# Kernel optimization log

Measured on AMD Instinct MI355X. Metric: run time of the kernel, lower is better.

Reference implementation:

```python
import jax, jax.numpy as jnp
import numpy as np

B, S, D_IN, D_MODEL, H = 2, 2048, 1024, 1024, 16
HD = D_MODEL // H


def setup_inputs() -> dict:
    key = jax.random.key(0)
    ks = jax.random.split(key, 5)
    x = jax.random.normal(ks[0], (B, S, D_IN), dtype=jnp.float32)
    # nn.Linear default init scale ~ 1/sqrt(fan_in)
    w_qkv = jax.random.normal(ks[1], (D_IN, 3 * D_MODEL), dtype=jnp.float32) / np.sqrt(D_IN)
    b_qkv = jax.random.normal(ks[2], (3 * D_MODEL,), dtype=jnp.float32) * 0.02
    w_out = jax.random.normal(ks[3], (D_MODEL, D_MODEL), dtype=jnp.float32) / np.sqrt(D_MODEL)
    b_out = jax.random.normal(ks[4], (D_MODEL,), dtype=jnp.float32) * 0.02
    return {"x": x, "w_qkv": w_qkv, "b_qkv": b_qkv, "w_out": w_out, "b_out": b_out}


def reference(x, w_qkv, b_qkv, w_out, b_out):
    b, s, _ = x.shape
    qkv = x @ w_qkv + b_qkv                       # [b, s, 3*d_model]
    # per-head layout is [q_h | k_h | v_h]: reshape to (b, s, h, 3, hd)
    qkv = qkv.reshape(b, s, H, 3, HD).transpose(0, 2, 1, 3, 4)  # [b, h, s, 3, hd]
    q, k, v = qkv[..., 0, :], qkv[..., 1, :], qkv[..., 2, :]     # each [b, h, s, hd]
    scale = 1.0 / np.sqrt(HD).astype(np.float32)
    scores = jnp.einsum('bhqd,bhkd->bhqk', q, k) * scale         # [b, h, s, s]
    causal = jnp.tril(jnp.ones((s, s), dtype=bool))              # True = keep
    scores = jnp.where(causal, scores, -jnp.inf)
    attn = jax.nn.softmax(scores, axis=-1)
    out = jnp.einsum('bhqk,bhkd->bhqd', attn, v)                 # [b, h, s, hd]
    concat = out.transpose(0, 2, 1, 3).reshape(b, s, D_MODEL)
    return concat @ w_out + b_out
```

## Files before the change

kernel.cpp:

```cpp
#include <hip/hip_runtime.h>
#include <hip/hip_bf16.h>
#include <stdint.h>

typedef __attribute__((ext_vector_type(8))) short bf16x8;
typedef __attribute__((ext_vector_type(4))) float f32x4;

#define DEVFN static __device__ __forceinline__

typedef const __attribute__((address_space(1))) void* gas_ptr;
typedef __attribute__((address_space(3))) void* las_ptr;

DEVFN void async16(const void* g, void* l) {
  __builtin_amdgcn_global_load_lds((gas_ptr)g, (las_ptr)l, 16, 0, 0);
}

#define S_LEN 2048
#define NH    16
#define HDIM  64
#define KDIM  1024
#define NQKV  3072
#define MTOK  4096

#define QK_SCALE 0.1803368801111244f

__global__ __launch_bounds__(256) void prep_kernel(
    const float* __restrict__ x, const float* __restrict__ w_qkv,
    const float* __restrict__ w_out, __hip_bfloat16* __restrict__ xb,
    __hip_bfloat16* __restrict__ wqkt, __hip_bfloat16* __restrict__ wot) {
  __shared__ float T[64][65];
  const int j = blockIdx.x;
  const int tid = threadIdx.x;
  if (j < 2048) {
    const int i = (j * 256 + tid) * 8;
    float4 a = *(const float4*)(x + i);
    float4 b = *(const float4*)(x + i + 4);
    alignas(16) __hip_bfloat16 t[8] = {
        __float2bfloat16(a.x), __float2bfloat16(a.y),
        __float2bfloat16(a.z), __float2bfloat16(a.w),
        __float2bfloat16(b.x), __float2bfloat16(b.y),
        __float2bfloat16(b.z), __float2bfloat16(b.w)};
    *(uint4*)(xb + i) = *(const uint4*)t;
    return;
  }
  const float* in;
  __hip_bfloat16* out;
  int N, n0, k0;
  if (j < 2816) {
    const int j2 = j - 2048;
    in = w_qkv; out = wqkt; N = NQKV;
    n0 = (j2 % 48) * 64; k0 = (j2 / 48) * 64;
  } else {
    const int j3 = j - 2816;
    in = w_out; out = wot; N = KDIM;
    n0 = (j3 % 16) * 64; k0 = (j3 / 16) * 64;
  }
#pragma unroll
  for (int it = 0; it < 4; it++) {
    int r = it * 16 + (tid >> 4);
    int c = (tid & 15) * 4;
    float4 v = *(const float4*)&in[(size_t)(k0 + r) * N + n0 + c];
    T[r][c + 0] = v.x; T[r][c + 1] = v.y; T[r][c + 2] = v.z; T[r][c + 3] = v.w;
  }
  __syncthreads();
#pragma unroll
  for (int it = 0; it < 4; it++) {
    int rn = it * 16 + (tid >> 4);
    int ck = (tid & 15) * 4;
    alignas(8) __hip_bfloat16 t4[4];
#pragma unroll
    for (int jj = 0; jj < 4; jj++) t4[jj] = __float2bfloat16(T[ck + jj][rn]);
    *(ushort4*)&out[(size_t)(n0 + rn) * KDIM + k0 + ck] = *(const ushort4*)t4;
  }
}

__global__ __launch_bounds__(256, 2) void qkv_gemm_kernel(
    const __hip_bfloat16* __restrict__ A,
    const __hip_bfloat16* __restrict__ Bt,
    const float* __restrict__ bias,
    __hip_bfloat16* __restrict__ qo,
    __hip_bfloat16* __restrict__ ko,
    __hip_bfloat16* __restrict__ vto) {
  __shared__ __hip_bfloat16 As[2][128 * 32];
  __shared__ __hip_bfloat16 Bs[2][128 * 32];
  __shared__ __hip_bfloat16 Tb[4][16 * 72];
  const int tid = threadIdx.x;
  const int wave = tid >> 6, lane = tid & 63;
  const int L = lane & 15, quad = lane >> 4;
  const int wm = wave >> 1, wn = wave & 1;
  const int m0 = blockIdx.y * 128, n0 = blockIdx.x * 128;

  f32x4 acc[4][4] = {};

  const int srow = tid >> 2;
  const int scol = (tid & 3) * 8;
  const __hip_bfloat16* ag = A + (size_t)(m0 + srow) * KDIM + scol;
  const __hip_bfloat16* bg = Bt + (size_t)(n0 + srow) * KDIM + scol;
  char* asd0 = (char*)&As[0][0] + wave * 1024;
  char* asd1 = (char*)&As[1][0] + wave * 1024;
  char* bsd0 = (char*)&Bs[0][0] + wave * 1024;
  char* bsd1 = (char*)&Bs[1][0] + wave * 1024;

  for (int kt = 0; kt < KDIM; kt += 64) {
    async16(ag + kt, asd0);
    async16(ag + kt + (size_t)64 * KDIM, asd0 + 4096);
    async16(ag + kt + 32, asd1);
    async16(ag + kt + 32 + (size_t)64 * KDIM, asd1 + 4096);
    async16(bg + kt, bsd0);
    async16(bg + kt + (size_t)64 * KDIM, bsd0 + 4096);
    async16(bg + kt + 32, bsd1);
    async16(bg + kt + 32 + (size_t)64 * KDIM, bsd1 + 4096);
    __syncthreads();
    bf16x8 af[4][2], bf[4][2];
#pragma unroll
    for (int r = 0; r < 4; r++)
#pragma unroll
      for (int kd = 0; kd < 2; kd++)
        af[r][kd] = *(const bf16x8*)&As[kd][(wm * 64 + r * 16 + L) * 32 + quad * 8];
#pragma unroll
    for (int c = 0; c < 4; c++)
#pragma unroll
      for (int kd = 0; kd < 2; kd++)
        bf[c][kd] = *(const bf16x8*)&Bs[kd][(wn * 64 + c * 16 + L) * 32 + quad * 8];
#pragma unroll
    for (int r = 0; r < 4; r++)
#pragma unroll
      for (int c = 0; c < 4; c++) {
        acc[r][c] = __builtin_amdgcn_mfma_f32_16x16x32_bf16(af[r][0], bf[c][0],
                                                            acc[r][c], 0, 0, 0);
        acc[r][c] = __builtin_amdgcn_mfma_f32_16x16x32_bf16(af[r][1], bf[c][1],
                                                            acc[r][c], 0, 0, 0);
      }
    __syncthreads();
  }

  const int mbase = m0 + wm * 64;
  const int nbase = n0 + wn * 64;
  const int h = nbase / 192;
  const int t = (nbase % 192) / 64;
  const int b = mbase >> 11;
  const int s0 = mbase & 2047;
  __hip_bfloat16* Tw = &Tb[wave][0];
  float bv[4];
#pragma unroll
  for (int c = 0; c < 4; c++) bv[c] = bias[nbase + c * 16 + L];

  if (t == 2) {
#pragma unroll
    for (int c = 0; c < 4; c++) {
#pragma unroll
      for (int r = 0; r < 4; r++) {
        alignas(8) __hip_bfloat16 t4[4];
#pragma unroll
        for (int g = 0; g < 4; g++)
          t4[g] = __float2bfloat16(acc[r][c][g] + bv[c]);
        *(ushort4*)&Tw[L * 72 + r * 16 + quad * 4] = *(const ushort4*)t4;
      }
      __asm__ volatile("s_waitcnt lgkmcnt(0)" ::: "memory");
#pragma unroll
      for (int it = 0; it < 2; it++) {
        const int rr = it * 8 + (lane >> 3);
        const int cc = (lane & 7) * 8;
        uint4 u = *(const uint4*)&Tw[rr * 72 + cc];
        *(uint4*)&vto[((size_t)((b * NH + h) * HDIM + c * 16 + rr)) * S_LEN +
                      s0 + cc] = u;
      }
    }
  } else {
    __hip_bfloat16* dst = (t == 0) ? qo : ko;
    const float sc = (t == 0) ? QK_SCALE : 1.0f;
#pragma unroll
    for (int r = 0; r < 4; r++) {
#pragma unroll
      for (int c = 0; c < 4; c++)
#pragma unroll
        for (int g = 0; g < 4; g++)
          Tw[(quad * 4 + g) * 72 + c * 16 + L] =
              __float2bfloat16((acc[r][c][g] + bv[c]) * sc);
      __asm__ volatile("s_waitcnt lgkmcnt(0)" ::: "memory");
#pragma unroll
      for (int it = 0; it < 2; it++) {
        const int rr = it * 8 + (lane >> 3);
        const int cc = (lane & 7) * 8;
        uint4 u = *(const uint4*)&Tw[rr * 72 + cc];
        *(uint4*)&dst[((size_t)((b * NH + h) * S_LEN) + s0 + r * 16 + rr) *
                          HDIM + cc] = u;
      }
    }
  }
}

__global__ __launch_bounds__(256, 2) void flash_attn_kernel(
    const __hip_bfloat16* __restrict__ q,
    const __hip_bfloat16* __restrict__ k,
    const __hip_bfloat16* __restrict__ vt,
    __hip_bfloat16* __restrict__ attn) {
  __shared__ __hip_bfloat16 Ps[4][16 * 72];
  const int tid = threadIdx.x;
  const int wave = tid >> 6, lane = tid & 63;
  const int L = lane & 15, quad = lane >> 4;

  const int j = blockIdx.x;
  const int x = j & 7;
  const int c = (j >> 3) & 31;
  const int rr = j >> 8;
  const int bh = ((c & 3) << 3) + x;
  const int p = c >> 2;
  const int qi = rr ? p : (15 - p);
  const int qb = qi * 128;

  const __hip_bfloat16* Qg = q + (size_t)bh * S_LEN * HDIM;
  const __hip_bfloat16* Kg = k + (size_t)bh * S_LEN * HDIM;
  const __hip_bfloat16* Vg = vt + (size_t)bh * HDIM * S_LEN;

  int wq[2];
  wq[0] = qb + wave * 16;
  wq[1] = qb + 64 + wave * 16;

  bf16x8 qf[2][2];
#pragma unroll
  for (int r = 0; r < 2; r++)
#pragma unroll
    for (int kd = 0; kd < 2; kd++)
      qf[r][kd] =
          *(const bf16x8*)&Qg[(size_t)(wq[r] + L) * HDIM + kd * 32 + quad * 8];

  float l_i[2] = {0.f, 0.f};
  f32x4 o[2][4] = {};

  bf16x8 kc[4][2], kn[4][2];
#pragma unroll
  for (int ks = 0; ks < 4; ks++)
#pragma unroll
    for (int kd = 0; kd < 2; kd++)
      kc[ks][kd] =
          *(const bf16x8*)&Kg[(size_t)(ks * 16 + L) * HDIM + kd * 32 + quad * 8];

  const int nkt = 2 * (qi + 1);
  for (int kt = 0; kt < nkt; kt++) {
    const int k0 = kt * 64;
    bf16x8 vfr[4][2];
#pragma unroll
    for (int dsb = 0; dsb < 4; dsb++)
#pragma unroll
      for (int kf = 0; kf < 2; kf++)
        vfr[dsb][kf] = *(const bf16x8*)&Vg[(size_t)(dsb * 16 + L) * S_LEN + k0 +
                                           kf * 32 + quad * 8];

    f32x4 st[2][4] = {};
#pragma unroll
    for (int r = 0; r < 2; r++)
#pragma unroll
      for (int ks = 0; ks < 4; ks++)
#pragma unroll
        for (int kd = 0; kd < 2; kd++)
          st[r][ks] = __builtin_amdgcn_mfma_f32_16x16x32_bf16(
              kc[ks][kd], qf[r][kd], st[r][ks], 0, 0, 0);

    if (kt + 1 < nkt) {
      const int k1 = k0 + 64;
#pragma unroll
      for (int ks = 0; ks < 4; ks++)
#pragma unroll
        for (int kd = 0; kd < 2; kd++)
          kn[ks][kd] = *(const bf16x8*)&Kg[(size_t)(k1 + ks * 16 + L) * HDIM +
                                           kd * 32 + quad * 8];
    }

#pragma unroll
    for (int r = 0; r < 2; r++) {
      if (k0 > wq[r] + 15) continue;
      const int qrow = wq[r] + L;
      if (k0 + 63 > wq[r]) {
#pragma unroll
        for (int ks = 0; ks < 4; ks++)
#pragma unroll
          for (int g = 0; g < 4; g++) {
            int kk = k0 + ks * 16 + quad * 4 + g;
            if (kk > qrow) st[r][ks][g] = -1e30f;
          }
      }
      float rs = 0.f;
#pragma unroll
      for (int ks = 0; ks < 4; ks++) {
        f32x4 pv;
#pragma unroll
        for (int g = 0; g < 4; g++) {
          pv[g] = __builtin_amdgcn_exp2f(st[r][ks][g]);
          rs += pv[g];
        }
        alignas(8) __hip_bfloat16 t4[4];
#pragma unroll
        for (int g = 0; g < 4; g++) t4[g] = __float2bfloat16(pv[g]);
        *(ushort4*)&Ps[wave][L * 72 + ks * 16 + quad * 4] = *(const ushort4*)t4;
      }
      l_i[r] += rs;
      __asm__ volatile("s_waitcnt lgkmcnt(0)" ::: "memory");
      bf16x8 pf[2];
#pragma unroll
      for (int kf = 0; kf < 2; kf++)
        pf[kf] = *(const bf16x8*)&Ps[wave][L * 72 + kf * 32 + quad * 8];
#pragma unroll
      for (int dsb = 0; dsb < 4; dsb++)
#pragma unroll
        for (int kf = 0; kf < 2; kf++)
          o[r][dsb] = __builtin_amdgcn_mfma_f32_16x16x32_bf16(
              vfr[dsb][kf], pf[kf], o[r][dsb], 0, 0, 0);
    }
#pragma unroll
    for (int ks = 0; ks < 4; ks++)
#pragma unroll
      for (int kd = 0; kd < 2; kd++) kc[ks][kd] = kn[ks][kd];
  }

  const int b = bh >> 4, h = bh & 15;
#pragma unroll
  for (int r = 0; r < 2; r++) {
    float rs = l_i[r];
    rs += __shfl_xor(rs, 16, 64);
    rs += __shfl_xor(rs, 32, 64);
    const float linv = 1.0f / rs;
#pragma unroll
    for (int dsb = 0; dsb < 4; dsb++) {
      alignas(8) __hip_bfloat16 t4[4];
#pragma unroll
      for (int g = 0; g < 4; g++)
        t4[g] = __float2bfloat16(o[r][dsb][g] * linv);
      *(ushort4*)&Ps[wave][L * 72 + dsb * 16 + quad * 4] = *(const ushort4*)t4;
    }
    __asm__ volatile("s_waitcnt lgkmcnt(0)" ::: "memory");
#pragma unroll
    for (int it = 0; it < 2; it++) {
      const int row = it * 8 + (lane >> 3);
      const int col = (lane & 7) * 8;
      uint4 u = *(const uint4*)&Ps[wave][row * 72 + col];
      *(uint4*)&attn[((size_t)(b * S_LEN + wq[r] + row)) * 1024 + h * 64 + col] = u;
    }
  }
}

__global__ __launch_bounds__(256, 2) void out_gemm_kernel(
    const __hip_bfloat16* __restrict__ A,
    const __hip_bfloat16* __restrict__ Bt,
    const float* __restrict__ bias,
    float* __restrict__ out) {
  __shared__ __hip_bfloat16 As[2][128 * 32];
  __shared__ __hip_bfloat16 Bs[2][64 * 32];
  __shared__ float Os[4][16 * 36];
  const int tid = threadIdx.x;
  const int wave = tid >> 6, lane = tid & 63;
  const int L = lane & 15, quad = lane >> 4;
  const int wm = wave >> 1, wn = wave & 1;
  const int m0 = blockIdx.y * 128, n0 = blockIdx.x * 64;

  f32x4 acc[4][2] = {};

  const int srow = tid >> 2;
  const int scol = (tid & 3) * 8;
  const __hip_bfloat16* ag = A + (size_t)(m0 + srow) * KDIM + scol;
  const __hip_bfloat16* bg = Bt + (size_t)(n0 + srow) * KDIM + scol;
  char* asd0 = (char*)&As[0][0] + wave * 1024;
  char* asd1 = (char*)&As[1][0] + wave * 1024;
  char* bsd0 = (char*)&Bs[0][0] + wave * 1024;
  char* bsd1 = (char*)&Bs[1][0] + wave * 1024;

  for (int kt = 0; kt < KDIM; kt += 64) {
    async16(ag + kt, asd0);
    async16(ag + kt + (size_t)64 * KDIM, asd0 + 4096);
    async16(ag + kt + 32, asd1);
    async16(ag + kt + 32 + (size_t)64 * KDIM, asd1 + 4096);
    async16(bg + kt, bsd0);
    async16(bg + kt + 32, bsd1);
    __syncthreads();
    bf16x8 af[4][2], bf[2][2];
#pragma unroll
    for (int r = 0; r < 4; r++)
#pragma unroll
      for (int kd = 0; kd < 2; kd++)
        af[r][kd] = *(const bf16x8*)&As[kd][(wm * 64 + r * 16 + L) * 32 + quad * 8];
#pragma unroll
    for (int c = 0; c < 2; c++)
#pragma unroll
      for (int kd = 0; kd < 2; kd++)
        bf[c][kd] = *(const bf16x8*)&Bs[kd][(wn * 32 + c * 16 + L) * 32 + quad * 8];
#pragma unroll
    for (int r = 0; r < 4; r++)
#pragma unroll
      for (int c = 0; c < 2; c++) {
        acc[r][c] = __builtin_amdgcn_mfma_f32_16x16x32_bf16(af[r][0], bf[c][0],
                                                            acc[r][c], 0, 0, 0);
        acc[r][c] = __builtin_amdgcn_mfma_f32_16x16x32_bf16(af[r][1], bf[c][1],
                                                            acc[r][c], 0, 0, 0);
      }
    __syncthreads();
  }

  float bv[2];
#pragma unroll
  for (int c = 0; c < 2; c++) bv[c] = bias[n0 + wn * 32 + c * 16 + L];
#pragma unroll
  for (int r = 0; r < 4; r++) {
#pragma unroll
    for (int c = 0; c < 2; c++)
#pragma unroll
      for (int g = 0; g < 4; g++)
        Os[wave][(quad * 4 + g) * 36 + c * 16 + L] = acc[r][c][g] + bv[c];
    __asm__ volatile("s_waitcnt lgkmcnt(0)" ::: "memory");
#pragma unroll
    for (int it = 0; it < 2; it++) {
      const int row = it * 8 + (lane >> 3);
      const int ncol = (lane & 7) * 4;
      float4 u = *(const float4*)&Os[wave][row * 36 + ncol];
      *(float4*)&out[(size_t)(m0 + wm * 64 + r * 16 + row) * 1024 + n0 +
                     wn * 32 + ncol] = u;
    }
  }
}

extern "C" void kernel_launch(void* const* d_in, const int* in_sizes, int n_in,
                              void* d_out, int out_size, void* d_ws, size_t ws_size,
                              hipStream_t stream) {
  const float* x     = (const float*)d_in[0];
  const float* w_qkv = (const float*)d_in[1];
  const float* b_qkv = (const float*)d_in[2];
  const float* w_out = (const float*)d_in[3];
  const float* b_out = (const float*)d_in[4];
  float* out = (float*)d_out;

  __hip_bfloat16* ws = (__hip_bfloat16*)d_ws;
  __hip_bfloat16* xb   = ws;
  __hip_bfloat16* wqkt = xb   + (size_t)4194304;
  __hip_bfloat16* wot  = wqkt + (size_t)3145728;
  __hip_bfloat16* qb   = wot  + (size_t)1048576;
  __hip_bfloat16* kb   = qb   + (size_t)4194304;
  __hip_bfloat16* vtb  = kb   + (size_t)4194304;
  __hip_bfloat16* attn = vtb  + (size_t)4194304;

  prep_kernel<<<3072, 256, 0, stream>>>(x, w_qkv, w_out, xb, wqkt, wot);
  qkv_gemm_kernel<<<dim3(NQKV / 128, MTOK / 128), 256, 0, stream>>>(
      xb, wqkt, b_qkv, qb, kb, vtb);
  flash_attn_kernel<<<512, 256, 0, stream>>>(qb, kb, vtb, attn);
  out_gemm_kernel<<<dim3(KDIM / 64, MTOK / 128), 256, 0, stream>>>(
      attn, wot, b_out, out);
}
```

Before: 194.0 us.

## Stage K and V tiles in double-buffered shared memory for block-wide reuse

Each wave used to load its own K and V fragments straight from global memory. Now the block loads each 64-key K/V tile once, cooperatively, through registers into double-buffered LDS, and waves read their fragments from LDS. QK^T is also computed only for the active row block, which skips fully masked work. This cuts redundant global and L2 traffic fourfold, at the cost of a block-wide __syncthreads per tile, extra LDS footprint and LDS read latency.

```diff
diff --git a/kernel.cpp b/kernel.cpp
--- a/kernel.cpp
+++ b/kernel.cpp
@@ -194,6 +194,8 @@
     const __hip_bfloat16* __restrict__ k,
     const __hip_bfloat16* __restrict__ vt,
     __hip_bfloat16* __restrict__ attn) {
+  __shared__ __hip_bfloat16 Ks[2][8 * 64 * 8];
+  __shared__ __hip_bfloat16 Vs[2][8 * 64 * 8];
   __shared__ __hip_bfloat16 Ps[4][16 * 72];
   const int tid = threadIdx.x;
   const int wave = tid >> 6, lane = tid & 63;
@@ -227,56 +229,69 @@
   float l_i[2] = {0.f, 0.f};
   f32x4 o[2][4] = {};
 
-  bf16x8 kc[4][2], kn[4][2];
-#pragma unroll
-  for (int ks = 0; ks < 4; ks++)
-#pragma unroll
-    for (int kd = 0; kd < 2; kd++)
-      kc[ks][kd] =
-          *(const bf16x8*)&Kg[(size_t)(ks * 16 + L) * HDIM + kd * 32 + quad * 8];
+  const int row32 = tid >> 3;
+  const int g8 = tid & 7;
+  uint4 kreg[2], vreg[2];
 
   const int nkt = 2 * (qi + 1);
+#pragma unroll
+  for (int pp = 0; pp < 2; pp++) {
+    kreg[pp] = *(const uint4*)&Kg[(size_t)(pp * 32 + row32) * HDIM + g8 * 8];
+    vreg[pp] = *(const uint4*)&Vg[(size_t)(pp * 32 + row32) * S_LEN + g8 * 8];
+  }
+#pragma unroll
+  for (int pp = 0; pp < 2; pp++) {
+    *(uint4*)&Ks[0][g8 * 512 + (pp * 32 + row32) * 8] = kreg[pp];
+    *(uint4*)&Vs[0][g8 * 512 + (pp * 32 + row32) * 8] = vreg[pp];
+  }
+  __syncthreads();
+
   for (int kt = 0; kt < nkt; kt++) {
     const int k0 = kt * 64;
-    bf16x8 vfr[4][2];
-#pragma unroll
-    for (int dsb = 0; dsb < 4; dsb++)
-#pragma unroll
-      for (int kf = 0; kf < 2; kf++)
-        vfr[dsb][kf] = *(const bf16x8*)&Vg[(size_t)(dsb * 16 + L) * S_LEN + k0 +
-                                           kf * 32 + quad * 8];
-
-    f32x4 st[2][4] = {};
-#pragma unroll
-    for (int r = 0; r < 2; r++)
-#pragma unroll
-      for (int ks = 0; ks < 4; ks++)
-#pragma unroll
-        for (int kd = 0; kd < 2; kd++)
-          st[r][ks] = __builtin_amdgcn_mfma_f32_16x16x32_bf16(
-              kc[ks][kd], qf[r][kd], st[r][ks], 0, 0, 0);
-
+    const int cur = kt & 1;
     if (kt + 1 < nkt) {
       const int k1 = k0 + 64;
 #pragma unroll
-      for (int ks = 0; ks < 4; ks++)
-#pragma unroll
-        for (int kd = 0; kd < 2; kd++)
-          kn[ks][kd] = *(const bf16x8*)&Kg[(size_t)(k1 + ks * 16 + L) * HDIM +
-                                           kd * 32 + quad * 8];
-    }
+      for (int pp = 0; pp < 2; pp++) {
+        kreg[pp] =
+            *(const uint4*)&Kg[(size_t)(k1 + pp * 32 + row32) * HDIM + g8 * 8];
+        vreg[pp] =
+            *(const uint4*)&Vg[(size_t)(pp * 32 + row32) * S_LEN + k1 + g8 * 8];
+      }
+    }
+
+    bf16x8 kfr[4][2], vfr[4][2];
+#pragma unroll
+    for (int ks = 0; ks < 4; ks++)
+#pragma unroll
+      for (int kd = 0; kd < 2; kd++)
+        kfr[ks][kd] =
+            *(const bf16x8*)&Ks[cur][(kd * 4 + quad) * 512 + (ks * 16 + L) * 8];
+#pragma unroll
+    for (int dsb = 0; dsb < 4; dsb++)
+#pragma unroll
+      for (int kf = 0; kf < 2; kf++)
+        vfr[dsb][kf] =
+            *(const bf16x8*)&Vs[cur][(kf * 4 + quad) * 512 + (dsb * 16 + L) * 8];
 
 #pragma unroll
     for (int r = 0; r < 2; r++) {
       if (k0 > wq[r] + 15) continue;
       const int qrow = wq[r] + L;
+      f32x4 st[4] = {};
+#pragma unroll
+      for (int ks = 0; ks < 4; ks++)
+#pragma unroll
+        for (int kd = 0; kd < 2; kd++)
+          st[ks] = __builtin_amdgcn_mfma_f32_16x16x32_bf16(
+              kfr[ks][kd], qf[r][kd], st[ks], 0, 0, 0);
       if (k0 + 63 > wq[r]) {
 #pragma unroll
         for (int ks = 0; ks < 4; ks++)
 #pragma unroll
           for (int g = 0; g < 4; g++) {
             int kk = k0 + ks * 16 + quad * 4 + g;
-            if (kk > qrow) st[r][ks][g] = -1e30f;
+            if (kk > qrow) st[ks][g] = -1e30f;
           }
       }
       float rs = 0.f;
@@ -285,7 +300,7 @@
         f32x4 pv;
 #pragma unroll
         for (int g = 0; g < 4; g++) {
-          pv[g] = __builtin_amdgcn_exp2f(st[r][ks][g]);
+          pv[g] = __builtin_amdgcn_exp2f(st[ks][g]);
           rs += pv[g];
         }
         alignas(8) __hip_bfloat16 t4[4];
@@ -306,10 +321,16 @@
           o[r][dsb] = __builtin_amdgcn_mfma_f32_16x16x32_bf16(
               vfr[dsb][kf], pf[kf], o[r][dsb], 0, 0, 0);
     }
-#pragma unroll
-    for (int ks = 0; ks < 4; ks++)
-#pragma unroll
-      for (int kd = 0; kd < 2; kd++) kc[ks][kd] = kn[ks][kd];
+
+    if (kt + 1 < nkt) {
+      const int nxt = cur ^ 1;
+#pragma unroll
+      for (int pp = 0; pp < 2; pp++) {
+        *(uint4*)&Ks[nxt][g8 * 512 + (pp * 32 + row32) * 8] = kreg[pp];
+        *(uint4*)&Vs[nxt][g8 * 512 + (pp * 32 + row32) * 8] = vreg[pp];
+      }
+      __syncthreads();
+    }
   }
 
   const int b = bh >> 4, h = bh & 15;
```

Result: faster. 182.7 us (-5.8%).
